# Optimization experiments

Measured on AMD Instinct MI355X. Metric: run time of the kernel, lower is better.

Reference implementation:

```python
import jax, jax.numpy as jnp
from jax import lax
import numpy as np

B, CIN, COUT, H, W, K = 4, 64, 64, 128, 128, 3
FACTOR = 2.0  # ivcf, tile != first-layer override path -> factor = ivcf
DN = ('NCHW', 'OIHW', 'NCHW')


def cimu_conv2d(x, weight, bias, factor):
    """Bit-serial int8 conv emulation: 8 bit-plane convs, per-plane clamp/round."""
    xq = jnp.clip(x, -128, 127).astype(jnp.int8).astype(jnp.uint8)  # two's complement bits
    shifts = jnp.arange(8, dtype=jnp.uint8).reshape(8, 1, 1, 1, 1)
    bits = ((xq[None] >> shifts) & jnp.uint8(1)).astype(jnp.float32)  # (8,B,C,Hp,Wp)
    P, b, c, hp, wp = bits.shape
    y = lax.conv_general_dilated(bits.reshape(P * b, c, hp, wp), weight,
                                 window_strides=(1, 1), padding='VALID',
                                 dimension_numbers=DN)  # (8B, Cout, Ho, Wo)
    y = y.reshape(P, b, y.shape[1], y.shape[2], y.shape[3])
    y = jnp.clip(jnp.round(y / factor), -128, 127)
    y = jnp.round(jnp.round(y * factor))
    plane_w = jnp.array([1., 2., 4., 8., 16., 32., 64., -128.], dtype=jnp.float32)
    y = jnp.einsum('pbchw,p->bchw', y, plane_w)
    return y + bias.reshape(1, -1, 1, 1)


def setup_inputs() -> dict:
    key = jax.random.key(0)
    ks = jax.random.split(key, 8)
    ri = lambda k, shape, lo, hi: (jax.random.randint(k, shape, lo, hi)).astype(jnp.float32)
    return {
        'cast_in':   ri(ks[0], (B, CIN, H, W), -128, 128),
        'merge_in':  ri(ks[1], (B, COUT, H, W), -128, 128),
        'gather_in': ri(ks[2], (B, COUT, H, W), -128, 128),
        'conv_weight': ri(ks[3], (COUT, CIN, K, K), -3, 4),
        'conv_bias':   ri(ks[4], (COUT,), -8, 8),
        'ctrans_i': ri(ks[5], (COUT,), 1, 4),            # per-channel integer multiplier
        'ctrans_s': jnp.full((COUT,), -1.0, jnp.float32),  # per-channel shift exponent
        'strans_i': jnp.float32(3.0),
        'strans_s': jnp.float32(-2.0),
        'atrans_i': jnp.float32(1.0),
        'atrans_s': jnp.float32(0.0),
    }


def reference(cast_in, merge_in, gather_in, conv_weight, conv_bias,
              ctrans_i, ctrans_s, strans_i, strans_s, atrans_i, atrans_s):
    # conv_pads = [1,1,1,1] (left,right,top,bottom on last two dims)
    x = jnp.pad(cast_in, ((0, 0), (0, 0), (1, 1), (1, 1)))
    x = cimu_conv2d(x, conv_weight, conv_bias, FACTOR)
    # merge add
    x = x + merge_in
    # merge-node quantize (hardtrans): mult = ctrans_i / 2^{-ctrans_s}
    cmult = (ctrans_i / (2.0 ** (-ctrans_s))).reshape(1, -1, 1, 1)
    x = jnp.clip(jnp.round(x * cmult), -128, 127)
    # gather add + quantize
    x = x + gather_in
    smult = strans_i / (2.0 ** (-strans_s))
    x = jnp.clip(jnp.round(x * smult), -128, 127)
    # Relu + quantize
    x = jax.nn.relu(x)
    amult = atrans_i / (2.0 ** (-atrans_s))
    x = jnp.clip(jnp.round(x * amult), -128, 127)
    # pool_pads = [0,0,0,0] (no-op), MaxPool 2x2 stride 2
    x = lax.reduce_window(x, -jnp.inf, lax.max, (1, 1, 2, 2), (1, 1, 2, 2), 'VALID')
    return x
```

## Files before the change

### kernel.cpp

```cpp
#include <hip/hip_runtime.h>
#include <cstdint>


typedef int i32x4  __attribute__((ext_vector_type(4)));
typedef int i32x16 __attribute__((ext_vector_type(16)));

#define XB_OFF   0u
#define XB_BYTES 4326400u
#define WPK_OFF  XB_BYTES
#define WPK_BYTES 36864u

__global__ __launch_bounds__(256) void k_stage(const float* __restrict__ s_cast,
                                               const float* __restrict__ wsrc,
                                               uint8_t* __restrict__ ws) {
  const int blk = blockIdx.x, t = threadIdx.x;
  if (blk >= 656) {
    const int hb = blk - 656;
    const int b = hb >> 1, r = (hb & 1) ? 129 : 0;
    uint8_t* base = ws + XB_OFF + ((size_t)(b * 130 + r) * 130) * 64;
    const uint4 z = {0, 0, 0, 0};
#pragma unroll
    for (int i = 0; i < 3; ++i) {
      const int s = i * 256 + t;
      if (s < 520) *(uint4*)(base + (size_t)s * 16) = z;
    }
    return;
  }
  if (blk >= 512) {
    const int idx = (blk - 512) * 256 + t;
    const int i = idx & 15, l = (idx >> 4) & 63, gg = (idx >> 10) & 1,
              c = idx >> 11;
    const int k = c * 32 + (l >> 5) * 16 + i;
    const int tap = k >> 6, ci = k & 63;
    const int kh = tap / 3, kw = tap % 3;
    const int cco = gg * 32 + (l & 31);
    const float wv = wsrc[((cco * 64 + ci) * 3 + kh) * 3 + kw];
    ((int8_t*)(ws + WPK_OFF))[idx] = (int8_t)(int)wv;
    return;
  }
  const int b = blk >> 7, h = blk & 127;
  __shared__ uint8_t lds[128 * 68];
  const float* s0 = s_cast + ((size_t)(b * 64) * 128 + h) * 128;
#pragma unroll
  for (int ci0 = 0; ci0 < 64; ci0 += 2) {
    const int ci = ci0 + (t >> 7), w = t & 127;
    const float v = s0[ci * 16384 + w];
    lds[w * 68 + ci] = (uint8_t)((int)v & 0xFF);
  }
  __syncthreads();
  uint8_t* row = ws + XB_OFF + (((size_t)b * 130 + h + 1) * 130) * 64;
#pragma unroll
  for (int j = 0; j < 8; ++j) {
    const int f = j * 256 + t;
    const int w = f >> 4, ci4 = f & 15;
    const uint32_t val = *(const uint32_t*)&lds[w * 68 + ci4 * 4];
    *(uint32_t*)(row + 64 + (size_t)f * 4) = val;
  }
  if (t < 8) {
    const int col = (t < 4) ? 0 : 129, seg = t & 3;
    const uint4 z = {0, 0, 0, 0};
    *(uint4*)(row + (size_t)col * 64 + seg * 16) = z;
  }
}

__global__ __launch_bounds__(256, 3) void k_main(
    const unsigned char* __restrict__ xb, const float* __restrict__ mgf,
    const float* __restrict__ gtf, const int8_t* __restrict__ wpk,
    const float* __restrict__ bias, const float* __restrict__ cti,
    const float* __restrict__ cts, const float* __restrict__ sti,
    const float* __restrict__ sts, const float* __restrict__ ati,
    const float* __restrict__ ats, float* __restrict__ outp) {
  const int tid = threadIdx.x, lane = tid & 63, wg = tid >> 6;
  const int blk = blockIdx.x;
  const int wq = blk & 7, ho = (blk >> 3) & 63, b = blk >> 9;
  const int h0 = ho * 2, w0 = wq * 16;

  __shared__ uint8_t ldsx[4 * 20 * 64];
  __shared__ i32x4 wpkl[2304];
  __shared__ uint8_t mgt8[2][2][64][20];
  __shared__ float po_lds[8][65];

#pragma unroll
  for (int i = 0; i < 2; ++i) {
    const int s = i * 256 + tid;
    if (s < 288) {
      const int row = s / 72, rm = s - row * 72;
      const int col = rm >> 2, ci16 = rm & 3;
      const uint4 v = *(const uint4*)(
          xb + ((size_t)((b * 130 + h0 + row) * 130) + w0 + col) * 64 + ci16 * 16);
      *(uint4*)(ldsx + (row * 20 + col) * 64 + ci16 * 16) = v;
    }
  }

#pragma unroll
  for (int i = 0; i < 9; ++i) {
    const int s = i * 256 + tid;
    wpkl[s] = *(const i32x4*)(wpk + (size_t)s * 16);
  }

#pragma unroll
  for (int which = 0; which < 2; ++which) {
    const float* sp = which ? gtf : mgf;
#pragma unroll
    for (int i = 0; i < 2; ++i) {
      const int slot = i * 256 + tid;
      const int co = slot >> 3, r3 = slot & 7, hh = r3 >> 2, seg = r3 & 3;
      const float4 v = *(const float4*)(
          sp + ((size_t)((b * 64 + co) * 128 + h0 + hh)) * 128 + w0 + seg * 4);
      const uint32_t pk =
          ((uint32_t)((int)v.x & 0xFF)) | ((uint32_t)((int)v.y & 0xFF) << 8) |
          ((uint32_t)((int)v.z & 0xFF) << 16) | ((uint32_t)((int)v.w & 0xFF) << 24);
      *(uint32_t*)&mgt8[which][hh][co][seg * 4] = pk;
    }
  }

  const int pix = (lane & 31) >> 3;
  const int plane = lane & 7;
  const int khalf = lane >> 5;
  const int dh = pix >> 1, dw = pix & 1;
  const uint8_t* lbw = ldsx + ((dh * 20) + (wg * 4 + dw)) * 64 + khalf * 16;

  const int col = lane & 31;
  const float bs0 = bias[col], bs1 = bias[col + 32];
  const float cm0 = ldexpf(cti[col], (int)cts[col]);
  const float cm1 = ldexpf(cti[col + 32], (int)cts[col + 32]);
  const float sm = ldexpf(sti[0], (int)sts[0]);
  const float am = ldexpf(ati[0], (int)ats[0]);
  float pwl[4];
  pwl[0] = khalf ? 16.f : 1.f;
  pwl[1] = khalf ? 32.f : 2.f;
  pwl[2] = khalf ? 64.f : 4.f;
  pwl[3] = khalf ? -128.f : 8.f;

  __syncthreads();

#define XOFF(c) ((((c) >> 1) / 3) * 1280 + (((c) >> 1) % 3) * 64 + ((c)&1) * 32)
  i32x16 acc[2][2] = {};
#pragma unroll
  for (int c = 0; c < 18; ++c) {
    const i32x4 B0 = wpkl[(c * 2 + 0) * 64 + lane];
    const i32x4 B1 = wpkl[(c * 2 + 1) * 64 + lane];
#pragma unroll
    for (int q = 0; q < 2; ++q) {
      const uint4 vv = *(const uint4*)(lbw + q * 128 + XOFF(c));
      i32x4 av;
      av[0] = (int)((vv.x >> plane) & 0x01010101u);
      av[1] = (int)((vv.y >> plane) & 0x01010101u);
      av[2] = (int)((vv.z >> plane) & 0x01010101u);
      av[3] = (int)((vv.w >> plane) & 0x01010101u);
      acc[q][0] = __builtin_amdgcn_mfma_i32_32x32x32_i8(av, B0, acc[q][0], 0, 0, 0);
      acc[q][1] = __builtin_amdgcn_mfma_i32_32x32x32_i8(av, B1, acc[q][1], 0, 0, 0);
    }
  }
#undef XOFF

#pragma unroll
  for (int q = 0; q < 2; ++q) {
    const int wol = wg * 2 + q;
#pragma unroll
    for (int gg = 0; gg < 2; ++gg) {
      const float bs = gg ? bs1 : bs0;
      const float cm = gg ? cm1 : cm0;
      const int cc = gg * 32 + col;
      float psum[4];
#pragma unroll
      for (int px = 0; px < 4; ++px) {
        float s = 0.f;
#pragma unroll
        for (int j = 0; j < 4; ++j) {
          const float y = (float)acc[q][gg][px * 4 + j];
          const float qq = fminf(fmaxf(rintf(y * 0.5f), -128.f), 127.f);
          s = fmaf(pwl[j], 2.f * qq, s);
        }
        psum[px] = s;
      }
#pragma unroll
      for (int px = 0; px < 4; ++px)
        psum[px] += __shfl_xor(psum[px], 32);

      float po = -3.0e38f;
#pragma unroll
      for (int px = 0; px < 4; ++px) {
        const int ww = wol * 2 + (px & 1);
        const int hh = px >> 1;
        const float mgv = (float)(int)(signed char)mgt8[0][hh][cc][ww];
        const float gtv = (float)(int)(signed char)mgt8[1][hh][cc][ww];
        const float x1 = psum[px] + bs + mgv;
        const float x2 = fminf(fmaxf(rintf(x1 * cm), -128.f), 127.f);
        const float x3 = x2 + gtv;
        const float x4 = fminf(fmaxf(rintf(x3 * sm), -128.f), 127.f);
        const float x5 = fmaxf(x4, 0.f);
        const float x6 = fminf(fmaxf(rintf(x5 * am), -128.f), 127.f);
        po = fmaxf(po, x6);
      }
      if (lane < 32)
        po_lds[wol][cc] = po;
    }
  }

  __syncthreads();
  {
    const int tco = tid >> 2, seg = tid & 3;
    float2 v;
    v.x = po_lds[seg * 2 + 0][tco];
    v.y = po_lds[seg * 2 + 1][tco];
    float* dst = outp + (((size_t)(b * 64 + tco)) * 64 + ho) * 64 + wq * 8 + seg * 2;
    *(float2*)dst = v;
  }
}

extern "C" void kernel_launch(void* const* d_in, const int* in_sizes, int n_in,
                              void* d_out, int out_size, void* d_ws, size_t ws_size,
                              hipStream_t stream) {
  const float* cast_in = (const float*)d_in[0];
  const float* merge_in = (const float*)d_in[1];
  const float* gather_in = (const float*)d_in[2];
  const float* conv_w = (const float*)d_in[3];
  const float* conv_b = (const float*)d_in[4];
  const float* cti = (const float*)d_in[5];
  const float* cts = (const float*)d_in[6];
  const float* sti = (const float*)d_in[7];
  const float* sts = (const float*)d_in[8];
  const float* ati = (const float*)d_in[9];
  const float* ats = (const float*)d_in[10];

  uint8_t* ws = (uint8_t*)d_ws;
  uint8_t* xb = ws + XB_OFF;
  int8_t* wpk = (int8_t*)(ws + WPK_OFF);

  k_stage<<<664, 256, 0, stream>>>(cast_in, conv_w, ws);
  k_main<<<2048, 256, 0, stream>>>(xb, merge_in, gather_in, wpk, conv_b, cti,
                                   cts, sti, sts, ati, ats, (float*)d_out);
}
```

Measured before the change: 35.93 us.

## Make k_main persistent over tiles with register-prefetched next-tile loads

The main kernel now launches 768 blocks that loop over the 2048 tiles. Packed weights are loaded into LDS once per block instead of once per tile. Each iteration prefetches the next tile's input, merge and gather data into registers while the current tile's MFMA loop and epilogue run. The price is extra registers and uneven tail work, since 2048 tiles over 768 blocks gives some blocks two tiles and others three.

```diff
diff --git a/kernel.cpp b/kernel.cpp
--- a/kernel.cpp
+++ b/kernel.cpp
@@ -71,9 +71,6 @@
     const float* __restrict__ sts, const float* __restrict__ ati,
     const float* __restrict__ ats, float* __restrict__ outp) {
   const int tid = threadIdx.x, lane = tid & 63, wg = tid >> 6;
-  const int blk = blockIdx.x;
-  const int wq = blk & 7, ho = (blk >> 3) & 63, b = blk >> 9;
-  const int h0 = ho * 2, w0 = wq * 16;
 
   __shared__ uint8_t ldsx[4 * 20 * 64];
   __shared__ i32x4 wpkl[2304];
@@ -81,38 +78,24 @@
   __shared__ float po_lds[8][65];
 
 #pragma unroll
-  for (int i = 0; i < 2; ++i) {
-    const int s = i * 256 + tid;
-    if (s < 288) {
-      const int row = s / 72, rm = s - row * 72;
-      const int col = rm >> 2, ci16 = rm & 3;
-      const uint4 v = *(const uint4*)(
-          xb + ((size_t)((b * 130 + h0 + row) * 130) + w0 + col) * 64 + ci16 * 16);
-      *(uint4*)(ldsx + (row * 20 + col) * 64 + ci16 * 16) = v;
-    }
-  }
-
-#pragma unroll
   for (int i = 0; i < 9; ++i) {
     const int s = i * 256 + tid;
     wpkl[s] = *(const i32x4*)(wpk + (size_t)s * 16);
   }
 
-#pragma unroll
-  for (int which = 0; which < 2; ++which) {
-    const float* sp = which ? gtf : mgf;
-#pragma unroll
-    for (int i = 0; i < 2; ++i) {
-      const int slot = i * 256 + tid;
-      const int co = slot >> 3, r3 = slot & 7, hh = r3 >> 2, seg = r3 & 3;
-      const float4 v = *(const float4*)(
-          sp + ((size_t)((b * 64 + co) * 128 + h0 + hh)) * 128 + w0 + seg * 4);
-      const uint32_t pk =
-          ((uint32_t)((int)v.x & 0xFF)) | ((uint32_t)((int)v.y & 0xFF) << 8) |
-          ((uint32_t)((int)v.z & 0xFF) << 16) | ((uint32_t)((int)v.w & 0xFF) << 24);
-      *(uint32_t*)&mgt8[which][hh][co][seg * 4] = pk;
-    }
-  }
+  const int xrow0 = tid / 72, xrm0 = tid - xrow0 * 72;
+  const int xcol0 = xrm0 >> 2, xci0 = xrm0 & 3;
+  uint8_t* const xw0 = ldsx + (xrow0 * 20 + xcol0) * 64 + xci0 * 16;
+  const int xs1 = 256 + tid;
+  const int xrow1 = xs1 / 72, xrm1 = xs1 - xrow1 * 72;
+  const int xcol1 = xrm1 >> 2, xci1 = xrm1 & 3;
+  uint8_t* const xw1 = ldsx + (xrow1 * 20 + xcol1) * 64 + xci1 * 16;
+  const int co0 = tid >> 3, hh0 = (tid & 7) >> 2, sg0 = tid & 3;
+  const int co1 = 32 + (tid >> 3);
+  uint32_t* const mw00 = (uint32_t*)&mgt8[0][hh0][co0][sg0 * 4];
+  uint32_t* const mw01 = (uint32_t*)&mgt8[0][hh0][co1][sg0 * 4];
+  uint32_t* const mw10 = (uint32_t*)&mgt8[1][hh0][co0][sg0 * 4];
+  uint32_t* const mw11 = (uint32_t*)&mgt8[1][hh0][co1][sg0 * 4];
 
   const int pix = (lane & 31) >> 3;
   const int plane = lane & 7;
@@ -132,80 +115,113 @@
   pwl[2] = khalf ? 64.f : 4.f;
   pwl[3] = khalf ? -128.f : 8.f;
 
-  __syncthreads();
+  uint4 xr0, xr1;
+  float4 m00, m01, m10, m11;
+  auto load_tile = [&](int T) {
+    const int wq_ = T & 7, ho_ = (T >> 3) & 63, b_ = T >> 9;
+    const int h0_ = ho_ * 2, w0_ = wq_ * 16;
+    xr0 = *(const uint4*)(
+        xb + ((size_t)((b_ * 130 + h0_ + xrow0) * 130) + w0_ + xcol0) * 64 + xci0 * 16);
+    if (tid < 32)
+      xr1 = *(const uint4*)(
+          xb + ((size_t)((b_ * 130 + h0_ + xrow1) * 130) + w0_ + xcol1) * 64 + xci1 * 16);
+    m00 = *(const float4*)(mgf + ((size_t)((b_ * 64 + co0) * 128 + h0_ + hh0)) * 128 + w0_ + sg0 * 4);
+    m01 = *(const float4*)(mgf + ((size_t)((b_ * 64 + co1) * 128 + h0_ + hh0)) * 128 + w0_ + sg0 * 4);
+    m10 = *(const float4*)(gtf + ((size_t)((b_ * 64 + co0) * 128 + h0_ + hh0)) * 128 + w0_ + sg0 * 4);
+    m11 = *(const float4*)(gtf + ((size_t)((b_ * 64 + co1) * 128 + h0_ + hh0)) * 128 + w0_ + sg0 * 4);
+  };
+  auto pack8 = [](const float4& v) -> uint32_t {
+    return ((uint32_t)((int)v.x & 0xFF)) | ((uint32_t)((int)v.y & 0xFF) << 8) |
+           ((uint32_t)((int)v.z & 0xFF) << 16) | ((uint32_t)((int)v.w & 0xFF) << 24);
+  };
+
+  load_tile(blockIdx.x);
+
+#pragma unroll 1
+  for (int t = blockIdx.x; t < 2048; t += 768) {
+    const int wq = t & 7, ho = (t >> 3) & 63, b = t >> 9;
+    __syncthreads();
+    *(uint4*)xw0 = xr0;
+    if (tid < 32) *(uint4*)xw1 = xr1;
+    *mw00 = pack8(m00);
+    *mw01 = pack8(m01);
+    *mw10 = pack8(m10);
+    *mw11 = pack8(m11);
+    if (t + 768 < 2048) load_tile(t + 768);
+    __syncthreads();
 
 #define XOFF(c) ((((c) >> 1) / 3) * 1280 + (((c) >> 1) % 3) * 64 + ((c)&1) * 32)
-  i32x16 acc[2][2] = {};
-#pragma unroll
-  for (int c = 0; c < 18; ++c) {
-    const i32x4 B0 = wpkl[(c * 2 + 0) * 64 + lane];
-    const i32x4 B1 = wpkl[(c * 2 + 1) * 64 + lane];
+    i32x16 acc[2][2] = {};
+#pragma unroll
+    for (int c = 0; c < 18; ++c) {
+      const i32x4 B0 = wpkl[(c * 2 + 0) * 64 + lane];
+      const i32x4 B1 = wpkl[(c * 2 + 1) * 64 + lane];
+#pragma unroll
+      for (int q = 0; q < 2; ++q) {
+        const uint4 vv = *(const uint4*)(lbw + q * 128 + XOFF(c));
+        i32x4 av;
+        av[0] = (int)((vv.x >> plane) & 0x01010101u);
+        av[1] = (int)((vv.y >> plane) & 0x01010101u);
+        av[2] = (int)((vv.z >> plane) & 0x01010101u);
+        av[3] = (int)((vv.w >> plane) & 0x01010101u);
+        acc[q][0] = __builtin_amdgcn_mfma_i32_32x32x32_i8(av, B0, acc[q][0], 0, 0, 0);
+        acc[q][1] = __builtin_amdgcn_mfma_i32_32x32x32_i8(av, B1, acc[q][1], 0, 0, 0);
+      }
+    }
+#undef XOFF
+
 #pragma unroll
     for (int q = 0; q < 2; ++q) {
-      const uint4 vv = *(const uint4*)(lbw + q * 128 + XOFF(c));
-      i32x4 av;
-      av[0] = (int)((vv.x >> plane) & 0x01010101u);
-      av[1] = (int)((vv.y >> plane) & 0x01010101u);
-      av[2] = (int)((vv.z >> plane) & 0x01010101u);
-      av[3] = (int)((vv.w >> plane) & 0x01010101u);
-      acc[q][0] = __builtin_amdgcn_mfma_i32_32x32x32_i8(av, B0, acc[q][0], 0, 0, 0);
-      acc[q][1] = __builtin_amdgcn_mfma_i32_32x32x32_i8(av, B1, acc[q][1], 0, 0, 0);
-    }
-  }
-#undef XOFF
-
-#pragma unroll
-  for (int q = 0; q < 2; ++q) {
-    const int wol = wg * 2 + q;
-#pragma unroll
-    for (int gg = 0; gg < 2; ++gg) {
-      const float bs = gg ? bs1 : bs0;
-      const float cm = gg ? cm1 : cm0;
-      const int cc = gg * 32 + col;
-      float psum[4];
-#pragma unroll
-      for (int px = 0; px < 4; ++px) {
-        float s = 0.f;
-#pragma unroll
-        for (int j = 0; j < 4; ++j) {
-          const float y = (float)acc[q][gg][px * 4 + j];
-          const float qq = fminf(fmaxf(rintf(y * 0.5f), -128.f), 127.f);
-          s = fmaf(pwl[j], 2.f * qq, s);
+      const int wol = wg * 2 + q;
+#pragma unroll
+      for (int gg = 0; gg < 2; ++gg) {
+        const float bs = gg ? bs1 : bs0;
+        const float cm = gg ? cm1 : cm0;
+        const int cc = gg * 32 + col;
+        float psum[4];
+#pragma unroll
+        for (int px = 0; px < 4; ++px) {
+          float s = 0.f;
+#pragma unroll
+          for (int j = 0; j < 4; ++j) {
+            const float y = (float)acc[q][gg][px * 4 + j];
+            const float qq = fminf(fmaxf(rintf(y * 0.5f), -128.f), 127.f);
+            s = fmaf(pwl[j], 2.f * qq, s);
+          }
+          psum[px] = s;
         }
-        psum[px] = s;
+#pragma unroll
+        for (int px = 0; px < 4; ++px)
+          psum[px] += __shfl_xor(psum[px], 32);
+
+        float po = -3.0e38f;
+#pragma unroll
+        for (int px = 0; px < 4; ++px) {
+          const int ww = wol * 2 + (px & 1);
+          const int hh = px >> 1;
+          const float mgv = (float)(int)(signed char)mgt8[0][hh][cc][ww];
+          const float gtv = (float)(int)(signed char)mgt8[1][hh][cc][ww];
+          const float x1 = psum[px] + bs + mgv;
+          const float x2 = fminf(fmaxf(rintf(x1 * cm), -128.f), 127.f);
+          const float x3 = x2 + gtv;
+          const float x4 = fminf(fmaxf(rintf(x3 * sm), -128.f), 127.f);
+          const float x5 = fmaxf(x4, 0.f);
+          const float x6 = fminf(fmaxf(rintf(x5 * am), -128.f), 127.f);
+          po = fmaxf(po, x6);
+        }
+        if (lane < 32) po_lds[wol][cc] = po;
       }
-#pragma unroll
-      for (int px = 0; px < 4; ++px)
-        psum[px] += __shfl_xor(psum[px], 32);
-
-      float po = -3.0e38f;
-#pragma unroll
-      for (int px = 0; px < 4; ++px) {
-        const int ww = wol * 2 + (px & 1);
-        const int hh = px >> 1;
-        const float mgv = (float)(int)(signed char)mgt8[0][hh][cc][ww];
-        const float gtv = (float)(int)(signed char)mgt8[1][hh][cc][ww];
-        const float x1 = psum[px] + bs + mgv;
-        const float x2 = fminf(fmaxf(rintf(x1 * cm), -128.f), 127.f);
-        const float x3 = x2 + gtv;
-        const float x4 = fminf(fmaxf(rintf(x3 * sm), -128.f), 127.f);
-        const float x5 = fmaxf(x4, 0.f);
-        const float x6 = fminf(fmaxf(rintf(x5 * am), -128.f), 127.f);
-        po = fmaxf(po, x6);
-      }
-      if (lane < 32)
-        po_lds[wol][cc] = po;
-    }
-  }
-
-  __syncthreads();
-  {
-    const int tco = tid >> 2, seg = tid & 3;
-    float2 v;
-    v.x = po_lds[seg * 2 + 0][tco];
-    v.y = po_lds[seg * 2 + 1][tco];
-    float* dst = outp + (((size_t)(b * 64 + tco)) * 64 + ho) * 64 + wq * 8 + seg * 2;
-    *(float2*)dst = v;
+    }
+
+    __syncthreads();
+    {
+      const int tco = tid >> 2, seg = tid & 3;
+      float2 v;
+      v.x = po_lds[seg * 2 + 0][tco];
+      v.y = po_lds[seg * 2 + 1][tco];
+      *(float2*)(outp + (((size_t)(b * 64 + tco)) * 64 + ho) * 64 + wq * 8 +
+                 seg * 2) = v;
+    }
   }
 }
 
@@ -229,6 +245,6 @@
   int8_t* wpk = (int8_t*)(ws + WPK_OFF);
 
   k_stage<<<664, 256, 0, stream>>>(cast_in, conv_w, ws);
-  k_main<<<2048, 256, 0, stream>>>(xb, merge_in, gather_in, wpk, conv_b, cti,
-                                   cts, sti, sts, ati, ats, (float*)d_out);
+  k_main<<<768, 256, 0, stream>>>(xb, merge_in, gather_in, wpk, conv_b, cti,
+                                  cts, sti, sts, ati, ats, (float*)d_out);
 }
```

Result: no change. 36.01 us (+0.2%).
